# Optimization experiments

Hardware: AMD Instinct MI355X
Metric: run time of the kernel (lower is better)

Reference implementation:

```python
import jax, jax.numpy as jnp
import numpy as np

B, T, D, R = 16, 4096, 512, 256

# Buffers (match torch: linspace(0,T-1,R).long() truncates toward zero)
_LANDMARKS = np.linspace(0.0, T - 1, R).astype(np.int64)
_POS = np.arange(T)[:, None]                                   # [T,1]
_MASK = (_LANDMARKS[None, :] < _POS)                           # [T,R] bool: landmark j < position i
_TDIST = np.clip((_POS.astype(np.float32) - _LANDMARKS[None, :].astype(np.float32)) / T, 0.0, None).astype(np.float32)  # [T,R]


def setup_inputs() -> dict:
    key = jax.random.key(0)
    k1, k2, k3 = jax.random.split(key, 3)
    return {
        "z": jax.random.normal(k1, (B, T, D), dtype=jnp.float32),
        "gegenbauer_weights": jax.random.normal(k2, (3,), dtype=jnp.float32),
        "temporal_alpha": jax.random.normal(k3, (1,), dtype=jnp.float32),
    }


def reference(z, gegenbauer_weights, temporal_alpha):
    dtype = z.dtype
    mask = jnp.asarray(_MASK)                       # [T,R]
    tdist = jnp.asarray(_TDIST, dtype=dtype)        # [T,R]
    lm = jnp.asarray(_LANDMARKS)                    # [R]

    # F.normalize(z, dim=-1) with eps=1e-12
    norm = jnp.linalg.norm(z, axis=-1, keepdims=True)
    Q = z / jnp.maximum(norm, 1e-12)                # [B,T,D]
    K = Q[:, lm, :]                                 # [B,R,D]
    C = jnp.einsum('btd,brd->btr', Q, K)            # [B,T,R] cosine similarity

    # Gegenbauer mixture
    alpha = jax.nn.softmax(gegenbauer_weights)
    C2 = C * C
    P1 = (1.0 + C) * 0.5
    P2 = (3.0 * C2 - 1.0) * 0.5
    P3 = (5.0 * C2 * C - 3.0 * C) * 0.5
    Phi = alpha[0] * P1 + alpha[1] * P2 + alpha[2] * P3

    # Causal mask
    Phi = Phi * mask.astype(dtype)[None, :, :]

    # Temporal decay
    a_td = jax.nn.softplus(temporal_alpha[0])
    Phi = Phi * jnp.exp(-a_td * tdist)[None, :, :]

    # Row-sum normalization
    row_sum = jnp.maximum(Phi.sum(axis=-1, keepdims=True), 1e-6)
    Phi = Phi / row_sum

    # Append constant-ones feature -> [B,T,R+1]
    ones = jnp.ones((Phi.shape[0], Phi.shape[1], 1), dtype=dtype)
    return jnp.concatenate([Phi, ones], axis=-1)
```

## Files before the change

kernel.cpp:

```cpp
#include <hip/hip_runtime.h>
#include <hip/hip_bf16.h>
#include <math.h>

#define B_DIM 16
#define T_DIM 4096
#define D_DIM 512
#define R_DIM 256

#define TM 64
#define BK 64
#define LDP 72
#define NKS (D_DIM/32)
#define THREADS 512

typedef __bf16 bf16x8 __attribute__((ext_vector_type(8)));
typedef float floatx4 __attribute__((ext_vector_type(4)));

__device__ __forceinline__ int landmark_of(int r) {
    if (r >= 255) return 4095;
    const double step = 4095.0 / 255.0;
    return (int)((double)r * step);
}

__device__ __forceinline__ void split_bf16(float x, __bf16& h, __bf16& l) {
    h = (__bf16)x;
    l = (__bf16)(x - (float)h);
}

__global__ void nystrom_prep_kernel(const float* __restrict__ z,
                                    __bf16* __restrict__ Khi, __bf16* __restrict__ Klo) {
    int blk = blockIdx.x;
    int b = blk >> 8;
    int r = blk & 255;
    int lane = threadIdx.x;
    int lm = landmark_of(r);
    const float* src = z + ((size_t)b * T_DIM + lm) * D_DIM + lane * 8;
    float4 v0 = ((const float4*)src)[0];
    float4 v1 = ((const float4*)src)[1];
    float ss = v0.x*v0.x + v0.y*v0.y + v0.z*v0.z + v0.w*v0.w
             + v1.x*v1.x + v1.y*v1.y + v1.z*v1.z + v1.w*v1.w;
    #pragma unroll
    for (int off = 1; off < 64; off <<= 1) ss += __shfl_xor(ss, off, 64);
    float inv = 1.0f / fmaxf(sqrtf(ss), 1e-12f);
    float q[8] = {v0.x*inv, v0.y*inv, v0.z*inv, v0.w*inv,
                  v1.x*inv, v1.y*inv, v1.z*inv, v1.w*inv};
    bf16x8 oh, ol;
    #pragma unroll
    for (int j = 0; j < 8; j++) { __bf16 h, l; split_bf16(q[j], h, l); oh[j] = h; ol[j] = l; }
    size_t dst = ((((size_t)b * NKS + (lane >> 2)) * 16 + (r >> 4)) * 64
                  + (size_t)(lane & 3) * 16 + (r & 15)) * 8;
    *(bf16x8*)(Khi + dst) = oh;
    *(bf16x8*)(Klo + dst) = ol;
}

template<int NACT>
__device__ __forceinline__ void mfma_phase(const __bf16* __restrict__ Ash,
                                           const __bf16* __restrict__ Asl,
                                           const __bf16* __restrict__ khp,
                                           const __bf16* __restrict__ klp,
                                           int koff, int ln, floatx4 (&acc)[4][2]) {
    bf16x8 bh[NACT], bl[NACT];
    #pragma unroll
    for (int ni = 0; ni < NACT; ni++) {
        bh[ni] = *(const bf16x8*)(khp + ni * 4096);
        bl[ni] = *(const bf16x8*)(klp + ni * 4096);
    }
    __builtin_amdgcn_s_setprio(1);
    #pragma unroll
    for (int mi = 0; mi < 4; mi++) {
        bf16x8 afh = *(const bf16x8*)&Ash[(mi * 16 + ln) * LDP + koff];
        bf16x8 afl = *(const bf16x8*)&Asl[(mi * 16 + ln) * LDP + koff];
        #pragma unroll
        for (int ni = 0; ni < NACT; ni++) {
            acc[mi][ni] = __builtin_amdgcn_mfma_f32_16x16x32_bf16(afh, bh[ni], acc[mi][ni], 0, 0, 0);
            acc[mi][ni] = __builtin_amdgcn_mfma_f32_16x16x32_bf16(afh, bl[ni], acc[mi][ni], 0, 0, 0);
            acc[mi][ni] = __builtin_amdgcn_mfma_f32_16x16x32_bf16(afl, bh[ni], acc[mi][ni], 0, 0, 0);
        }
    }
    __builtin_amdgcn_s_setprio(0);
}

__global__ __launch_bounds__(THREADS, 4)
void nystrom_main_kernel(const float* __restrict__ z,
                         const __bf16* __restrict__ Khi, const __bf16* __restrict__ Klo,
                         const float* __restrict__ gw, const float* __restrict__ ta,
                         float* __restrict__ out) {
    __shared__ __attribute__((aligned(16))) char smem[36864];
    __shared__ int   lmtab[R_DIM];
    __shared__ float elmtab[R_DIM];

    float* red    = (float*)(smem);
    float* rnormp = (float*)(smem + 2048);
    float* rinvp  = (float*)(smem + 2304);
    float* rspart = (float*)(smem + 2560);

    const int tid  = threadIdx.x;
    const int bid  = blockIdx.x;
    const int b    = bid & 15;
    const int t0   = (bid >> 4) * TM;
    const int lane = tid & 63;
    const int wv   = tid >> 6;
    const int quad = lane >> 4;
    const int ln   = lane & 15;

    float g0 = gw[0], g1 = gw[1], g2 = gw[2];
    float gm = fmaxf(g0, fmaxf(g1, g2));
    float e0 = expf(g0 - gm), e1 = expf(g1 - gm), e2 = expf(g2 - gm);
    float esum = e0 + e1 + e2;
    float al0 = e0 / esum, al1 = e1 / esum, al2 = e2 / esum;
    float ax = ta[0];
    float a_td = (ax > 20.f) ? ax : log1pf(expf(ax));

    if (tid < R_DIM) {
        int lm = landmark_of(tid);
        lmtab[tid] = lm;
        elmtab[tid] = expf(a_td * (float)lm * (1.0f / 4096.0f));
    }

    int nact = 0;
    #pragma unroll
    for (int ni = 0; ni < 2; ni++)
        if (landmark_of(ni * 128 + wv * 16) < t0 + TM - 1) nact = ni + 1;

    const int srowA = tid >> 3;
    const int scolA = (tid & 7) * 8;
    const float* zrow = z + ((size_t)b * T_DIM + (t0 + srowA)) * D_DIM + scolA;

    const size_t kfoff = (size_t)b * (NKS * 16 * 64 * 8)
                       + (size_t)wv * 512 + (size_t)lane * 8;
    const __bf16* khb = Khi + kfoff;
    const __bf16* klb = Klo + kfoff;

    floatx4 acc[4][2];
    #pragma unroll
    for (int i = 0; i < 4; i++)
        #pragma unroll
        for (int j = 0; j < 2; j++) acc[i][j] = (floatx4){0.f, 0.f, 0.f, 0.f};
    float ssq = 0.0f;

    float4 a0, a1;

    {
        const float4* ap = (const float4*)(zrow);
        a0 = ap[0]; a1 = ap[1];
        float av[8] = {a0.x,a0.y,a0.z,a0.w, a1.x,a1.y,a1.z,a1.w};
        #pragma unroll
        for (int j = 0; j < 8; j++) ssq += av[j] * av[j];
        bf16x8 ph, pl;
        #pragma unroll
        for (int j = 0; j < 8; j++) { __bf16 h, l; split_bf16(av[j], h, l); ph[j] = h; pl[j] = l; }
        *(bf16x8*)&((__bf16*)(smem))[srowA * LDP + scolA] = ph;
        *(bf16x8*)&((__bf16*)(smem + 9216))[srowA * LDP + scolA] = pl;
    }
    __syncthreads();

    #pragma unroll 1
    for (int kt = 0; kt < D_DIM; kt += BK) {
        const int cur = (kt >> 6) & 1;
        const bool has_next = (kt + BK < D_DIM);

        if (has_next) {
            const float4* ap = (const float4*)(zrow + kt + BK);
            a0 = ap[0]; a1 = ap[1];
        }

        const __bf16* Ash = (const __bf16*)(smem + cur * 18432);
        const __bf16* Asl = (const __bf16*)(smem + cur * 18432 + 9216);
        const int ksb = kt >> 5;
        #pragma unroll
        for (int s = 0; s < 2; s++) {
            const __bf16* khp = khb + (size_t)(ksb + s) * 8192;
            const __bf16* klp = klb + (size_t)(ksb + s) * 8192;
            const int koff = s * 32 + quad * 8;
            switch (nact) {
                case 2: mfma_phase<2>(Ash, Asl, khp, klp, koff, ln, acc); break;
                case 1: mfma_phase<1>(Ash, Asl, khp, klp, koff, ln, acc); break;
                default: break;
            }
        }

        if (has_next) {
            float av[8] = {a0.x,a0.y,a0.z,a0.w, a1.x,a1.y,a1.z,a1.w};
            #pragma unroll
            for (int j = 0; j < 8; j++) ssq += av[j] * av[j];
            bf16x8 ph, pl;
            #pragma unroll
            for (int j = 0; j < 8; j++) { __bf16 h, l; split_bf16(av[j], h, l); ph[j] = h; pl[j] = l; }
            *(bf16x8*)&((__bf16*)(smem + (cur ^ 1) * 18432))[srowA * LDP + scolA] = ph;
            *(bf16x8*)&((__bf16*)(smem + (cur ^ 1) * 18432 + 9216))[srowA * LDP + scolA] = pl;
        }
        __syncthreads();
    }

    red[tid] = ssq;
    __syncthreads();
    if (tid < TM) {
        float s = 0.f;
        #pragma unroll
        for (int j = 0; j < 8; j++) s += red[tid * 8 + j];
        rnormp[tid] = 1.0f / fmaxf(sqrtf(s), 1e-12f);
    }
    __syncthreads();

    int   lm_r[2];
    float elm_r[2];
    #pragma unroll
    for (int ni = 0; ni < 2; ni++) {
        int r = ni * 128 + wv * 16 + ln;
        lm_r[ni]  = lmtab[r];
        elm_r[ni] = elmtab[r];
    }

    #pragma unroll
    for (int mi = 0; mi < 4; mi++) {
        #pragma unroll
        for (int reg = 0; reg < 4; reg++) {
            int row = mi * 16 + quad * 4 + reg;
            int t = t0 + row;
            float rn = rnormp[row];
            float e_t = __expf(-a_td * (float)t * (1.0f / 4096.0f));
            float s = 0.f;
            #pragma unroll
            for (int ni = 0; ni < 2; ni++) {
                float phi = 0.f;
                if (lm_r[ni] < t) {
                    float c  = acc[mi][ni][reg] * rn;
                    float c2 = c * c;
                    float P1 = 0.5f * (1.f + c);
                    float P2 = 0.5f * (3.f * c2 - 1.f);
                    float P3 = 0.5f * (5.f * c2 * c - 3.f * c);
                    float p  = al0 * P1 + al1 * P2 + al2 * P3;
                    phi = p * e_t * elm_r[ni];
                }
                acc[mi][ni][reg] = phi;
                s += phi;
            }
            #pragma unroll
            for (int off = 1; off < 16; off <<= 1) s += __shfl_xor(s, off, 64);
            if (ln == 0) rspart[wv * TM + row] = s;
        }
    }
    __syncthreads();
    if (tid < TM) {
        float rs = 0.f;
        #pragma unroll
        for (int w = 0; w < 8; w++) rs += rspart[w * TM + tid];
        rinvp[tid] = 1.0f / fmaxf(rs, 1e-6f);
    }
    __syncthreads();

    float* ob = out + ((size_t)b * T_DIM + t0) * 257;
    #pragma unroll
    for (int mi = 0; mi < 4; mi++) {
        #pragma unroll
        for (int reg = 0; reg < 4; reg++) {
            int row = mi * 16 + quad * 4 + reg;
            float inv = rinvp[row];
            #pragma unroll
            for (int ni = 0; ni < 2; ni++) {
                int r = ni * 128 + wv * 16 + ln;
                ob[(size_t)row * 257 + r] = acc[mi][ni][reg] * inv;
            }
        }
    }
    if (tid < TM) ob[(size_t)tid * 257 + 256] = 1.0f;
}

extern "C" void kernel_launch(void* const* d_in, const int* in_sizes, int n_in,
                              void* d_out, int out_size, void* d_ws, size_t ws_size,
                              hipStream_t stream) {
    const float* z  = (const float*)d_in[0];
    const float* gw = (const float*)d_in[1];
    const float* ta = (const float*)d_in[2];
    float* out = (float*)d_out;
    __bf16* Khi = (__bf16*)d_ws;
    __bf16* Klo = (__bf16*)((char*)d_ws + (size_t)B_DIM * R_DIM * D_DIM * 2);

    nystrom_prep_kernel<<<dim3(B_DIM * R_DIM), 64, 0, stream>>>(z, Khi, Klo);
    nystrom_main_kernel<<<dim3((T_DIM / TM) * B_DIM), THREADS, 0, stream>>>(z, Khi, Klo, gw, ta, out);
}
```

Measured before the change: 264.5 us.

## Stage full-row A tile in LDS once and run unrolled K chain without syncs

Replaces the double-buffered 64-wide K loop with a single upfront load of the entire 64x512 z tile, split into bf16 hi/lo halves in LDS, followed by one fully unrolled MFMA chain over all 16 K-steps. This removes the per-step barriers and the interleaved staging work. In exchange, LDS use rises to about 137 KB per block and launch bounds drop to 2 blocks per CU, so occupancy and the overlap of global loads with compute both fall. Each thread also holds 16 float4 registers in flight, which adds register pressure.

New measurement: 290.3 us. 9.8% more time.

```diff
diff --git a/kernel.cpp b/kernel.cpp
--- a/kernel.cpp
+++ b/kernel.cpp
@@ -8,10 +8,10 @@
 #define R_DIM 256
 
 #define TM 64
-#define BK 64
-#define LDP 72
+#define LDPA 536
 #define NKS (D_DIM/32)
 #define THREADS 512
+#define ASIZE (TM * LDPA * 2)
 
 typedef __bf16 bf16x8 __attribute__((ext_vector_type(8)));
 typedef float floatx4 __attribute__((ext_vector_type(4)));
@@ -54,38 +54,44 @@
 }
 
 template<int NACT>
-__device__ __forceinline__ void mfma_phase(const __bf16* __restrict__ Ash,
-                                           const __bf16* __restrict__ Asl,
-                                           const __bf16* __restrict__ khp,
-                                           const __bf16* __restrict__ klp,
-                                           int koff, int ln, floatx4 (&acc)[4][2]) {
-    bf16x8 bh[NACT], bl[NACT];
-    #pragma unroll
-    for (int ni = 0; ni < NACT; ni++) {
-        bh[ni] = *(const bf16x8*)(khp + ni * 4096);
-        bl[ni] = *(const bf16x8*)(klp + ni * 4096);
-    }
-    __builtin_amdgcn_s_setprio(1);
-    #pragma unroll
-    for (int mi = 0; mi < 4; mi++) {
-        bf16x8 afh = *(const bf16x8*)&Ash[(mi * 16 + ln) * LDP + koff];
-        bf16x8 afl = *(const bf16x8*)&Asl[(mi * 16 + ln) * LDP + koff];
+__device__ __forceinline__ void kchain(const __bf16* __restrict__ Ash,
+                                       const __bf16* __restrict__ Asl,
+                                       const __bf16* __restrict__ khb,
+                                       const __bf16* __restrict__ klb,
+                                       int quad, int ln, floatx4 (&acc)[4][2]) {
+    #pragma unroll
+    for (int s = 0; s < 16; s++) {
+        const __bf16* khp = khb + s * 8192;
+        const __bf16* klp = klb + s * 8192;
+        bf16x8 bh[NACT], bl[NACT];
         #pragma unroll
         for (int ni = 0; ni < NACT; ni++) {
-            acc[mi][ni] = __builtin_amdgcn_mfma_f32_16x16x32_bf16(afh, bh[ni], acc[mi][ni], 0, 0, 0);
-            acc[mi][ni] = __builtin_amdgcn_mfma_f32_16x16x32_bf16(afh, bl[ni], acc[mi][ni], 0, 0, 0);
-            acc[mi][ni] = __builtin_amdgcn_mfma_f32_16x16x32_bf16(afl, bh[ni], acc[mi][ni], 0, 0, 0);
-        }
-    }
-    __builtin_amdgcn_s_setprio(0);
-}
-
-__global__ __launch_bounds__(THREADS, 4)
+            bh[ni] = *(const bf16x8*)(khp + ni * 4096);
+            bl[ni] = *(const bf16x8*)(klp + ni * 4096);
+        }
+        const int koff = s * 32 + quad * 8;
+        __builtin_amdgcn_s_setprio(1);
+        #pragma unroll
+        for (int mi = 0; mi < 4; mi++) {
+            bf16x8 afh = *(const bf16x8*)&Ash[(mi * 16 + ln) * LDPA + koff];
+            bf16x8 afl = *(const bf16x8*)&Asl[(mi * 16 + ln) * LDPA + koff];
+            #pragma unroll
+            for (int ni = 0; ni < NACT; ni++) {
+                acc[mi][ni] = __builtin_amdgcn_mfma_f32_16x16x32_bf16(afh, bh[ni], acc[mi][ni], 0, 0, 0);
+                acc[mi][ni] = __builtin_amdgcn_mfma_f32_16x16x32_bf16(afh, bl[ni], acc[mi][ni], 0, 0, 0);
+                acc[mi][ni] = __builtin_amdgcn_mfma_f32_16x16x32_bf16(afl, bh[ni], acc[mi][ni], 0, 0, 0);
+            }
+        }
+        __builtin_amdgcn_s_setprio(0);
+    }
+}
+
+__global__ __launch_bounds__(THREADS, 2)
 void nystrom_main_kernel(const float* __restrict__ z,
                          const __bf16* __restrict__ Khi, const __bf16* __restrict__ Klo,
                          const float* __restrict__ gw, const float* __restrict__ ta,
                          float* __restrict__ out) {
-    __shared__ __attribute__((aligned(16))) char smem[36864];
+    __shared__ __attribute__((aligned(16))) char smem[2 * ASIZE];
     __shared__ int   lmtab[R_DIM];
     __shared__ float elmtab[R_DIM];
 
@@ -123,7 +129,7 @@
         if (landmark_of(ni * 128 + wv * 16) < t0 + TM - 1) nact = ni + 1;
 
     const int srowA = tid >> 3;
-    const int scolA = (tid & 7) * 8;
+    const int scolA = (tid & 7) * 64;
     const float* zrow = z + ((size_t)b * T_DIM + (t0 + srowA)) * D_DIM + scolA;
 
     const size_t kfoff = (size_t)b * (NKS * 16 * 64 * 8)
@@ -136,61 +142,40 @@
     for (int i = 0; i < 4; i++)
         #pragma unroll
         for (int j = 0; j < 2; j++) acc[i][j] = (floatx4){0.f, 0.f, 0.f, 0.f};
+
+    float4 az[16];
+    #pragma unroll
+    for (int j = 0; j < 16; j++) az[j] = ((const float4*)zrow)[j];
+
     float ssq = 0.0f;
-
-    float4 a0, a1;
-
     {
-        const float4* ap = (const float4*)(zrow);
-        a0 = ap[0]; a1 = ap[1];
-        float av[8] = {a0.x,a0.y,a0.z,a0.w, a1.x,a1.y,a1.z,a1.w};
-        #pragma unroll
-        for (int j = 0; j < 8; j++) ssq += av[j] * av[j];
-        bf16x8 ph, pl;
-        #pragma unroll
-        for (int j = 0; j < 8; j++) { __bf16 h, l; split_bf16(av[j], h, l); ph[j] = h; pl[j] = l; }
-        *(bf16x8*)&((__bf16*)(smem))[srowA * LDP + scolA] = ph;
-        *(bf16x8*)&((__bf16*)(smem + 9216))[srowA * LDP + scolA] = pl;
-    }
-    __syncthreads();
-
-    #pragma unroll 1
-    for (int kt = 0; kt < D_DIM; kt += BK) {
-        const int cur = (kt >> 6) & 1;
-        const bool has_next = (kt + BK < D_DIM);
-
-        if (has_next) {
-            const float4* ap = (const float4*)(zrow + kt + BK);
-            a0 = ap[0]; a1 = ap[1];
-        }
-
-        const __bf16* Ash = (const __bf16*)(smem + cur * 18432);
-        const __bf16* Asl = (const __bf16*)(smem + cur * 18432 + 9216);
-        const int ksb = kt >> 5;
-        #pragma unroll
-        for (int s = 0; s < 2; s++) {
-            const __bf16* khp = khb + (size_t)(ksb + s) * 8192;
-            const __bf16* klp = klb + (size_t)(ksb + s) * 8192;
-            const int koff = s * 32 + quad * 8;
-            switch (nact) {
-                case 2: mfma_phase<2>(Ash, Asl, khp, klp, koff, ln, acc); break;
-                case 1: mfma_phase<1>(Ash, Asl, khp, klp, koff, ln, acc); break;
-                default: break;
-            }
-        }
-
-        if (has_next) {
-            float av[8] = {a0.x,a0.y,a0.z,a0.w, a1.x,a1.y,a1.z,a1.w};
+        __bf16* Ash = (__bf16*)(smem);
+        __bf16* Asl = (__bf16*)(smem + ASIZE);
+        #pragma unroll
+        for (int c = 0; c < 8; c++) {
+            float av[8] = {az[2*c].x, az[2*c].y, az[2*c].z, az[2*c].w,
+                           az[2*c+1].x, az[2*c+1].y, az[2*c+1].z, az[2*c+1].w};
             #pragma unroll
             for (int j = 0; j < 8; j++) ssq += av[j] * av[j];
             bf16x8 ph, pl;
             #pragma unroll
             for (int j = 0; j < 8; j++) { __bf16 h, l; split_bf16(av[j], h, l); ph[j] = h; pl[j] = l; }
-            *(bf16x8*)&((__bf16*)(smem + (cur ^ 1) * 18432))[srowA * LDP + scolA] = ph;
-            *(bf16x8*)&((__bf16*)(smem + (cur ^ 1) * 18432 + 9216))[srowA * LDP + scolA] = pl;
-        }
-        __syncthreads();
-    }
+            *(bf16x8*)&Ash[srowA * LDPA + scolA + c * 8] = ph;
+            *(bf16x8*)&Asl[srowA * LDPA + scolA + c * 8] = pl;
+        }
+    }
+    __syncthreads();
+
+    {
+        const __bf16* Ash = (const __bf16*)(smem);
+        const __bf16* Asl = (const __bf16*)(smem + ASIZE);
+        switch (nact) {
+            case 2: kchain<2>(Ash, Asl, khb, klb, quad, ln, acc); break;
+            case 1: kchain<1>(Ash, Asl, khb, klb, quad, ln, acc); break;
+            default: break;
+        }
+    }
+    __syncthreads();
 
     red[tid] = ssq;
     __syncthreads();
```

## Software-pipeline K-fragment loads and prefetch z two tiles ahead in GEMM loop

Applied to the files above, without the earlier changes.

Restructures the D-reduction loop into per-NACT templated loops. B fragments (Khi/Klo) are now loaded into registers one substep ahead of their MFMA use, and z rows are prefetched two tiles ahead instead of one, to hide global-load latency behind MFMA work. The nact switch moves out of the inner loop. Launch bounds are relaxed from 4 to 3 blocks per SM to make room for the extra live registers, which may lower occupancy.

Measured after the change: 262.1 us. Within noise of the previous version (-0.9%).

```diff
diff --git a/kernel.cpp b/kernel.cpp
--- a/kernel.cpp
+++ b/kernel.cpp
@@ -54,17 +54,24 @@
 }
 
 template<int NACT>
-__device__ __forceinline__ void mfma_phase(const __bf16* __restrict__ Ash,
-                                           const __bf16* __restrict__ Asl,
-                                           const __bf16* __restrict__ khp,
-                                           const __bf16* __restrict__ klp,
-                                           int koff, int ln, floatx4 (&acc)[4][2]) {
-    bf16x8 bh[NACT], bl[NACT];
+__device__ __forceinline__ void ldB(const __bf16* __restrict__ khb,
+                                    const __bf16* __restrict__ klb, int g,
+                                    bf16x8 (&bh)[NACT], bf16x8 (&bl)[NACT]) {
+    const __bf16* khp = khb + (size_t)g * 8192;
+    const __bf16* klp = klb + (size_t)g * 8192;
     #pragma unroll
     for (int ni = 0; ni < NACT; ni++) {
         bh[ni] = *(const bf16x8*)(khp + ni * 4096);
         bl[ni] = *(const bf16x8*)(klp + ni * 4096);
     }
+}
+
+template<int NACT>
+__device__ __forceinline__ void mfma_step(const __bf16* __restrict__ Ash,
+                                          const __bf16* __restrict__ Asl,
+                                          int koff, int ln,
+                                          const bf16x8 (&bh)[NACT], const bf16x8 (&bl)[NACT],
+                                          floatx4 (&acc)[4][2]) {
     __builtin_amdgcn_s_setprio(1);
     #pragma unroll
     for (int mi = 0; mi < 4; mi++) {
@@ -80,7 +87,85 @@
     __builtin_amdgcn_s_setprio(0);
 }
 
-__global__ __launch_bounds__(THREADS, 4)
+__device__ __forceinline__ void stageA(char* smem, int buf, int srowA, int scolA,
+                                       const float4& z0, const float4& z1, float& ssq) {
+    float av[8] = {z0.x,z0.y,z0.z,z0.w, z1.x,z1.y,z1.z,z1.w};
+    #pragma unroll
+    for (int j = 0; j < 8; j++) ssq += av[j] * av[j];
+    bf16x8 ph, pl;
+    #pragma unroll
+    for (int j = 0; j < 8; j++) { __bf16 h, l; split_bf16(av[j], h, l); ph[j] = h; pl[j] = l; }
+    __bf16* Ash = (__bf16*)(smem + buf * 18432);
+    __bf16* Asl = (__bf16*)(smem + buf * 18432 + 9216);
+    *(bf16x8*)&Ash[srowA * LDP + scolA] = ph;
+    *(bf16x8*)&Asl[srowA * LDP + scolA] = pl;
+}
+
+template<int NACT>
+__device__ __forceinline__ void kloop(const float* __restrict__ zrow,
+                                      const __bf16* __restrict__ khb,
+                                      const __bf16* __restrict__ klb,
+                                      char* smem, int srowA, int scolA, int quad, int ln,
+                                      floatx4 (&acc)[4][2], float& ssq) {
+    bf16x8 bhc[NACT], blc[NACT], bhn[NACT], bln[NACT];
+    ldB<NACT>(khb, klb, 0, bhc, blc);
+    ldB<NACT>(khb, klb, 1, bhn, bln);
+    float4 zc0, zc1, zn0, zn1;
+    {
+        const float4* ap = (const float4*)zrow;
+        float4 t0 = ap[0], t1 = ap[1];
+        const float4* ap1 = (const float4*)(zrow + BK);
+        zc0 = ap1[0]; zc1 = ap1[1];
+        stageA(smem, 0, srowA, scolA, t0, t1, ssq);
+    }
+    __syncthreads();
+    #pragma unroll 1
+    for (int it = 0; it < 8; it++) {
+        const int cur = it & 1;
+        const __bf16* Ash = (const __bf16*)(smem + cur * 18432);
+        const __bf16* Asl = (const __bf16*)(smem + cur * 18432 + 9216);
+        if (it < 6) {
+            const float4* ap = (const float4*)(zrow + (it + 2) * BK);
+            zn0 = ap[0]; zn1 = ap[1];
+        }
+        mfma_step<NACT>(Ash, Asl, quad * 8,      ln, bhc, blc, acc);
+        if (it < 7) ldB<NACT>(khb, klb, 2 * it + 2, bhc, blc);
+        mfma_step<NACT>(Ash, Asl, 32 + quad * 8, ln, bhn, bln, acc);
+        if (it < 7) ldB<NACT>(khb, klb, 2 * it + 3, bhn, bln);
+        if (it < 7) {
+            stageA(smem, cur ^ 1, srowA, scolA, zc0, zc1, ssq);
+            zc0 = zn0; zc1 = zn1;
+        }
+        __syncthreads();
+    }
+}
+
+__device__ __forceinline__ void kloop0(const float* __restrict__ zrow,
+                                       char* smem, int srowA, int scolA, float& ssq) {
+    float4 zc0, zc1, zn0, zn1;
+    {
+        const float4* ap = (const float4*)zrow;
+        float4 t0 = ap[0], t1 = ap[1];
+        const float4* ap1 = (const float4*)(zrow + BK);
+        zc0 = ap1[0]; zc1 = ap1[1];
+        stageA(smem, 0, srowA, scolA, t0, t1, ssq);
+    }
+    __syncthreads();
+    #pragma unroll 1
+    for (int it = 0; it < 8; it++) {
+        if (it < 6) {
+            const float4* ap = (const float4*)(zrow + (it + 2) * BK);
+            zn0 = ap[0]; zn1 = ap[1];
+        }
+        if (it < 7) {
+            stageA(smem, (it & 1) ^ 1, srowA, scolA, zc0, zc1, ssq);
+            zc0 = zn0; zc1 = zn1;
+        }
+        __syncthreads();
+    }
+}
+
+__global__ __launch_bounds__(THREADS, 3)
 void nystrom_main_kernel(const float* __restrict__ z,
                          const __bf16* __restrict__ Khi, const __bf16* __restrict__ Klo,
                          const float* __restrict__ gw, const float* __restrict__ ta,
@@ -138,58 +223,10 @@
         for (int j = 0; j < 2; j++) acc[i][j] = (floatx4){0.f, 0.f, 0.f, 0.f};
     float ssq = 0.0f;
 
-    float4 a0, a1;
-
-    {
-        const float4* ap = (const float4*)(zrow);
-        a0 = ap[0]; a1 = ap[1];
-        float av[8] = {a0.x,a0.y,a0.z,a0.w, a1.x,a1.y,a1.z,a1.w};
-        #pragma unroll
-        for (int j = 0; j < 8; j++) ssq += av[j] * av[j];
-        bf16x8 ph, pl;
-        #pragma unroll
-        for (int j = 0; j < 8; j++) { __bf16 h, l; split_bf16(av[j], h, l); ph[j] = h; pl[j] = l; }
-        *(bf16x8*)&((__bf16*)(smem))[srowA * LDP + scolA] = ph;
-        *(bf16x8*)&((__bf16*)(smem + 9216))[srowA * LDP + scolA] = pl;
-    }
-    __syncthreads();
-
-    #pragma unroll 1
-    for (int kt = 0; kt < D_DIM; kt += BK) {
-        const int cur = (kt >> 6) & 1;
-        const bool has_next = (kt + BK < D_DIM);
-
-        if (has_next) {
-            const float4* ap = (const float4*)(zrow + kt + BK);
-            a0 = ap[0]; a1 = ap[1];
-        }
-
-        const __bf16* Ash = (const __bf16*)(smem + cur * 18432);
-        const __bf16* Asl = (const __bf16*)(smem + cur * 18432 + 9216);
-        const int ksb = kt >> 5;
-        #pragma unroll
-        for (int s = 0; s < 2; s++) {
-            const __bf16* khp = khb + (size_t)(ksb + s) * 8192;
-            const __bf16* klp = klb + (size_t)(ksb + s) * 8192;
-            const int koff = s * 32 + quad * 8;
-            switch (nact) {
-                case 2: mfma_phase<2>(Ash, Asl, khp, klp, koff, ln, acc); break;
-                case 1: mfma_phase<1>(Ash, Asl, khp, klp, koff, ln, acc); break;
-                default: break;
-            }
-        }
-
-        if (has_next) {
-            float av[8] = {a0.x,a0.y,a0.z,a0.w, a1.x,a1.y,a1.z,a1.w};
-            #pragma unroll
-            for (int j = 0; j < 8; j++) ssq += av[j] * av[j];
-            bf16x8 ph, pl;
-            #pragma unroll
-            for (int j = 0; j < 8; j++) { __bf16 h, l; split_bf16(av[j], h, l); ph[j] = h; pl[j] = l; }
-            *(bf16x8*)&((__bf16*)(smem + (cur ^ 1) * 18432))[srowA * LDP + scolA] = ph;
-            *(bf16x8*)&((__bf16*)(smem + (cur ^ 1) * 18432 + 9216))[srowA * LDP + scolA] = pl;
-        }
-        __syncthreads();
+    switch (nact) {
+        case 2: kloop<2>(zrow, khb, klb, smem, srowA, scolA, quad, ln, acc, ssq); break;
+        case 1: kloop<1>(zrow, khb, klb, smem, srowA, scolA, quad, ln, acc, ssq); break;
+        default: kloop0(zrow, smem, srowA, scolA, ssq); break;
     }
 
     red[tid] = ssq;
```
